# Kernel tuning notes

Measured on AMD Instinct MI355X. Metric: run time of the kernel, lower is better.

The kernel has to match this reference:

```python
import jax, jax.numpy as jnp
import numpy as np

HEADS = 3
NEG_SLOPE = 0.2


def setup_inputs() -> dict:
    key = jax.random.key(0)
    ks = jax.random.split(key, 16)
    B, node_num, his, in_dim = 2, 5000, 12, 2
    N = B * node_num
    E = 160000
    hidden = 32
    C = hidden * his  # 384, per-head out channels of GATConv
    gat_in = in_dim * his  # 24
    s = 0.05
    return {
        "x": jax.random.normal(ks[0], (B, node_num, his, in_dim), jnp.float32),
        "edge_index": jax.random.randint(ks[1], (2, E), 0, N, jnp.int64),
        "lin_w": jax.random.normal(ks[2], (HEADS * C, gat_in), jnp.float32) * s,
        "att_src": jax.random.normal(ks[3], (HEADS, C), jnp.float32) * s,
        "att_dst": jax.random.normal(ks[4], (HEADS, C), jnp.float32) * s,
        "gat_bias": jax.random.normal(ks[5], (C,), jnp.float32) * s,
        "w_ih": jax.random.normal(ks[6], (3 * hidden, hidden), jnp.float32) * s,
        "w_hh": jax.random.normal(ks[7], (3 * hidden, hidden), jnp.float32) * s,
        "b_ih": jax.random.normal(ks[8], (3 * hidden,), jnp.float32) * s,
        "b_hh": jax.random.normal(ks[9], (3 * hidden,), jnp.float32) * s,
        "p1_w": jax.random.normal(ks[10], (1, hidden), jnp.float32) * s,
        "p1_b": jax.random.normal(ks[11], (1,), jnp.float32) * s,
        "p2_w": jax.random.normal(ks[12], (his, his), jnp.float32) * s,
        "p2_b": jax.random.normal(ks[13], (his,), jnp.float32) * s,
    }


def _gat_conv(xf, src, dst, N, lin_w, att_src, att_dst, gat_bias):
    # xf: [N, gat_in]; returns [N, C] (mean over heads, concat=False)
    heads, C = att_src.shape
    h = (xf @ lin_w.T).reshape(N, heads, C)           # [N,heads,C]
    a_src = jnp.einsum('nhc,hc->nh', h, att_src)      # [N,heads]
    a_dst = jnp.einsum('nhc,hc->nh', h, att_dst)
    alpha = jax.nn.leaky_relu(a_src[src] + a_dst[dst], NEG_SLOPE)  # [E,heads]
    # edge softmax over incoming edges of each dst node (stable)
    amax = jax.ops.segment_max(alpha, dst, num_segments=N)
    ea = jnp.exp(alpha - amax[dst])
    denom = jax.ops.segment_sum(ea, dst, num_segments=N)
    w = ea / denom[dst]                               # [E,heads]
    msg = h[src] * w[:, :, None]                      # [E,heads,C] -- dominant traffic
    out = jax.ops.segment_sum(msg, dst, num_segments=N)
    return out.mean(axis=1) + gat_bias                # [N,C]


def _gru(seq, w_ih, w_hh, b_ih, b_hh):
    # seq: [N, T, H] -> outputs [N, T, H], PyTorch GRU gate order (r,z,n)
    N, T, H = seq.shape
    def step(hprev, xt):
        gi = xt @ w_ih.T + b_ih
        gh = hprev @ w_hh.T + b_hh
        ir, iz, inn = jnp.split(gi, 3, axis=-1)
        hr, hz, hn = jnp.split(gh, 3, axis=-1)
        r = jax.nn.sigmoid(ir + hr)
        z = jax.nn.sigmoid(iz + hz)
        n = jnp.tanh(inn + r * hn)
        hnew = (1.0 - z) * n + z * hprev
        return hnew, hnew
    h0 = jnp.zeros((N, H), seq.dtype)
    _, hs = jax.lax.scan(step, h0, seq.transpose(1, 0, 2))
    return hs.transpose(1, 0, 2)


def reference(x, edge_index, lin_w, att_src, att_dst, gat_bias,
              w_ih, w_hh, b_ih, b_hh, p1_w, p1_b, p2_w, p2_b):
    B, node_num, his, in_dim = x.shape
    N = B * node_num
    xf = x.reshape(N, his * in_dim)
    # GATConv adds self-loops (add_self_loops=True default in PyG)
    loops = jnp.arange(N)
    src = jnp.concatenate([edge_index[0], loops])
    dst = jnp.concatenate([edge_index[1], loops])
    gat_out = _gat_conv(xf, src, dst, N, lin_w, att_src, att_dst, gat_bias)  # [N, hidden*his]
    hidden = w_hh.shape[1]
    gru_in = gat_out.reshape(N, his, hidden)
    gru_out = _gru(gru_in, w_ih, w_hh, b_ih, b_hh)    # [N, his, hidden]
    o = (gru_out @ p1_w.T + p1_b).squeeze(-1)         # [N, his]
    o = o @ p2_w.T + p2_b                              # [N, pred_num]
    return o.reshape(B, node_num, -1)
```

## Files before the change

### kernel.cpp

```cpp
#include <hip/hip_runtime.h>
#include <math.h>

#define HEADS 3
#define C_OUT 384
#define GAT_IN 24
#define HID 32
#define TSTEPS 12
#define NEG_SLOPE 0.2f
#define CAPW 64
#define SLOTS 96

typedef __attribute__((ext_vector_type(8))) short bf16x8;
typedef __attribute__((ext_vector_type(4))) float f32x4;

__device__ __forceinline__ float sigm(float x) {
  return 1.f / (1.f + __expf(-x));
}
__device__ __forceinline__ float tanh_fast(float x) {
  return 2.f / (1.f + __expf(-2.f * x)) - 1.f;
}
__device__ __forceinline__ unsigned short f2bf(float x) {
  unsigned int u = __float_as_uint(x);
  unsigned int r = u + 0x7fffu + ((u >> 16) & 1u);
  return (unsigned short)(r >> 16);
}
__device__ __forceinline__ float bf2f(unsigned short u) {
  return __uint_as_float((unsigned int)u << 16);
}
__device__ __forceinline__ float lrelu(float x) {
  return x >= 0.f ? x : NEG_SLOPE * x;
}

__global__ __launch_bounds__(96) void k_const(const float* __restrict__ lin_w,
                                              const float* __restrict__ gat_bias,
                                              const float* __restrict__ wih,
                                              const float* __restrict__ bih,
                                              const float* __restrict__ att_src,
                                              const float* __restrict__ att_dst,
                                              unsigned short* __restrict__ WWt,
                                              float* __restrict__ biasb,
                                              float* __restrict__ vbuf,
                                              int* __restrict__ cnt, int N) {
  int b = blockIdx.x;
  if (b < 876) {
    int t = b / 73, k = b % 73;
    int g = threadIdx.x;
    __shared__ float s_w[32];
    if (g < 32) {
      if (k < 72) {
        int h = k / 24, j = k % 24;
        s_w[g] = lin_w[(size_t)(h * C_OUT + t * 32 + g) * GAT_IN + j] * (1.f / 3.f);
      } else {
        s_w[g] = gat_bias[t * 32 + g];
      }
    }
    __syncthreads();
    const float* wrow = wih + (size_t)g * 32;
    float acc = 0.f;
#pragma unroll
    for (int c = 0; c < 32; ++c) acc += s_w[c] * wrow[c];
    if (k < 72) {
      WWt[((size_t)t * 96 + g) * 96 + k] = f2bf(acc);
      if (k < 24) WWt[((size_t)t * 96 + g) * 96 + 72 + k] = 0;
    } else {
      biasb[t * 96 + g] = acc + bih[g];
    }
  } else if (b < 948) {
    int bb = b - 876;
    int h = bb / 24, j = bb % 24;
    int lane = threadIdx.x;
    if (lane >= 64) return;
    float as = 0.f, ad = 0.f;
    for (int c = lane; c < C_OUT; c += 64) {
      float wv = lin_w[(size_t)(h * C_OUT + c) * GAT_IN + j];
      as += att_src[h * C_OUT + c] * wv;
      ad += att_dst[h * C_OUT + c] * wv;
    }
#pragma unroll
    for (int off = 32; off >= 1; off >>= 1) {
      as += __shfl_xor(as, off, 64);
      ad += __shfl_xor(ad, off, 64);
    }
    if (lane == 0) {
      vbuf[h * 24 + j] = as;
      vbuf[72 + h * 24 + j] = ad;
    }
  } else {
    int i = (b - 948) * 96 + threadIdx.x;
    if (i < N) cnt[i] = 0;
  }
}

__global__ void k_place(const int* __restrict__ esrc,
                        const int* __restrict__ edst, int* __restrict__ cnt,
                        int* __restrict__ slist, int E, int ET) {
  int e = blockIdx.x * blockDim.x + threadIdx.x;
  if (e >= ET) return;
  int d, s;
  if (e < E) { d = edst[e]; s = esrc[e]; }
  else { d = e - E; s = e - E; }
  int pos = atomicAdd(&cnt[d], 1);
  if (pos < SLOTS) slist[(size_t)d * SLOTS + pos] = s;
}

__global__ __launch_bounds__(256) void k_aggx(
    const float* __restrict__ xf, const float* __restrict__ vbuf,
    const int* __restrict__ slist, const int* __restrict__ cnt,
    unsigned short* __restrict__ Yb, int N) {
  __shared__ float s_v[144];
  __shared__ float s_w[4][CAPW][3];
  __shared__ unsigned short s_xb[4][CAPW][26];
  int tid = threadIdx.x, lane = tid & 63, wv = tid >> 6;
  if (tid < 144) s_v[tid] = vbuf[tid];
  __syncthreads();
  int n = blockIdx.x * 4 + wv;
  if (n >= N) return;

  int deg = min(cnt[n], SLOTS);

  float xl = (lane < 24) ? xf[(size_t)n * 24 + lane] : 0.f;
  float ad0, ad1, ad2;
  {
    float p0 = (lane < 24) ? xl * s_v[72 + lane] : 0.f;
    float p1 = (lane < 24) ? xl * s_v[96 + lane] : 0.f;
    float p2 = (lane < 24) ? xl * s_v[120 + lane] : 0.f;
#pragma unroll
    for (int off = 32; off >= 1; off >>= 1) {
      p0 += __shfl_xor(p0, off, 64);
      p1 += __shfl_xor(p1, off, 64);
      p2 += __shfl_xor(p2, off, 64);
    }
    ad0 = p0; ad1 = p1; ad2 = p2;
  }

  float t0 = 0.f, t1 = 0.f, t2 = 0.f;
  for (int i = lane; i < deg; i += 64) {
    int s = slist[(size_t)n * SLOTS + i];
    const float4* xr = (const float4*)(xf + (size_t)s * 24);
    float xs[24];
#pragma unroll
    for (int q = 0; q < 6; ++q) {
      float4 v = xr[q];
      xs[4 * q] = v.x; xs[4 * q + 1] = v.y;
      xs[4 * q + 2] = v.z; xs[4 * q + 3] = v.w;
    }
    float as0 = 0.f, as1 = 0.f, as2 = 0.f;
#pragma unroll
    for (int j = 0; j < 24; ++j) {
      float v = xs[j];
      as0 += v * s_v[j];
      as1 += v * s_v[24 + j];
      as2 += v * s_v[48 + j];
    }
    float e0 = __expf(lrelu(as0 + ad0));
    float e1 = __expf(lrelu(as1 + ad1));
    float e2 = __expf(lrelu(as2 + ad2));
    if (i < CAPW) {
      s_w[wv][i][0] = e0; s_w[wv][i][1] = e1; s_w[wv][i][2] = e2;
#pragma unroll
      for (int j = 0; j < 24; ++j) s_xb[wv][i][j] = f2bf(xs[j]);
    }
    t0 += e0; t1 += e1; t2 += e2;
  }
#pragma unroll
  for (int off = 32; off >= 1; off >>= 1) {
    t0 += __shfl_xor(t0, off, 64);
    t1 += __shfl_xor(t1, off, 64);
    t2 += __shfl_xor(t2, off, 64);
  }
  float inv0 = 1.f / t0, inv1 = 1.f / t1, inv2 = 1.f / t2;

  int eg = lane >> 5;
  int c = lane & 31;
  float acc0 = 0.f, acc1 = 0.f, acc2 = 0.f;
  if (deg <= CAPW) {
    int cc = (c < 24) ? c : 0;
    float cmask = (c < 24) ? 1.f : 0.f;
#pragma unroll 2
    for (int i = eg; i < deg; i += 2) {
      float w0 = s_w[wv][i][0] * inv0;
      float w1 = s_w[wv][i][1] * inv1;
      float w2 = s_w[wv][i][2] * inv2;
      float xv = bf2f(s_xb[wv][i][cc]) * cmask;
      acc0 += w0 * xv; acc1 += w1 * xv; acc2 += w2 * xv;
    }
  } else {
    for (int i = eg; i < deg; i += 2) {
      int s = slist[(size_t)n * SLOTS + i];
      float as0 = 0.f, as1 = 0.f, as2 = 0.f;
      const float* xr = xf + (size_t)s * 24;
#pragma unroll
      for (int j = 0; j < 24; ++j) {
        float v = xr[j];
        as0 += v * s_v[j];
        as1 += v * s_v[24 + j];
        as2 += v * s_v[48 + j];
      }
      float w0 = __expf(lrelu(as0 + ad0)) * inv0;
      float w1 = __expf(lrelu(as1 + ad1)) * inv1;
      float w2 = __expf(lrelu(as2 + ad2)) * inv2;
      float xv = (c < 24) ? xf[(size_t)s * 24 + c] : 0.f;
      acc0 += w0 * xv; acc1 += w1 * xv; acc2 += w2 * xv;
    }
  }
  acc0 += __shfl_xor(acc0, 32, 64);
  acc1 += __shfl_xor(acc1, 32, 64);
  acc2 += __shfl_xor(acc2, 32, 64);
  if (lane < 24) {
    unsigned short* yr = Yb + (size_t)n * 72;
    yr[lane] = f2bf(acc0);
    yr[24 + lane] = f2bf(acc1);
    yr[48 + lane] = f2bf(acc2);
  }
}

__global__ __launch_bounds__(64) void k_rec2(
    const unsigned short* __restrict__ Yb,
    const unsigned short* __restrict__ WWt, const float* __restrict__ biasb,
    const float* __restrict__ whh, const float* __restrict__ bhh,
    const float* __restrict__ p1w, const float* __restrict__ p1b,
    const float* __restrict__ p2w, const float* __restrict__ p2b,
    float* __restrict__ out, int N) {
  __shared__ unsigned short h16[16][32];
  __shared__ float s_o[16][12];
  int l = threadIdx.x;
  int c = l & 15, hi = l >> 4;
  int m0 = blockIdx.x * 16;

  int row = min(m0 + c, N - 1);
  const unsigned short* yr = Yb + (size_t)row * 72;
  bf16x8 ya0 = *(const bf16x8*)(yr + hi * 8);
  bf16x8 ya1 = *(const bf16x8*)(yr + 32 + hi * 8);
  bf16x8 ya2 = {0, 0, 0, 0, 0, 0, 0, 0};
  if (hi == 0) ya2 = *(const bf16x8*)(yr + 64);

  bf16x8 wb[6];
#pragma unroll
  for (int nt = 0; nt < 6; ++nt) {
    const float* wp = whh + (size_t)(nt * 16 + c) * 32 + hi * 8;
#pragma unroll
    for (int j = 0; j < 8; ++j) wb[nt][j] = (short)f2bf(wp[j]);
  }

  float bhr0 = bhh[c], bhr1 = bhh[c + 16];
  float bhz0 = bhh[32 + c], bhz1 = bhh[48 + c];
  float bhn0 = bhh[64 + c], bhn1 = bhh[80 + c];
  float p1c0 = p1w[c], p1c1 = p1w[c + 16], p1b0 = p1b[0];

  float hA[4] = {0.f, 0.f, 0.f, 0.f}, hB[4] = {0.f, 0.f, 0.f, 0.f};
  bf16x8 ha = {0, 0, 0, 0, 0, 0, 0, 0};

  for (int t = 0; t < TSTEPS; ++t) {
    const unsigned short* Wt = WWt + (size_t)t * 96 * 96;
    f32x4 g0 = {0,0,0,0}, g1 = {0,0,0,0}, g2 = {0,0,0,0};
    f32x4 g3 = {0,0,0,0}, g4 = {0,0,0,0}, g5 = {0,0,0,0};
#pragma unroll
    for (int q = 0; q < 3; ++q) {
      bf16x8 aq = (q == 0) ? ya0 : (q == 1) ? ya1 : ya2;
      int ko = q * 32 + hi * 8;
      bf16x8 b0 = *(const bf16x8*)(Wt + (size_t)(0 * 16 + c) * 96 + ko);
      bf16x8 b1 = *(const bf16x8*)(Wt + (size_t)(1 * 16 + c) * 96 + ko);
      bf16x8 b2 = *(const bf16x8*)(Wt + (size_t)(2 * 16 + c) * 96 + ko);
      bf16x8 b3 = *(const bf16x8*)(Wt + (size_t)(3 * 16 + c) * 96 + ko);
      bf16x8 b4 = *(const bf16x8*)(Wt + (size_t)(4 * 16 + c) * 96 + ko);
      bf16x8 b5 = *(const bf16x8*)(Wt + (size_t)(5 * 16 + c) * 96 + ko);
      g0 = __builtin_amdgcn_mfma_f32_16x16x32_bf16(aq, b0, g0, 0, 0, 0);
      g1 = __builtin_amdgcn_mfma_f32_16x16x32_bf16(aq, b1, g1, 0, 0, 0);
      g2 = __builtin_amdgcn_mfma_f32_16x16x32_bf16(aq, b2, g2, 0, 0, 0);
      g3 = __builtin_amdgcn_mfma_f32_16x16x32_bf16(aq, b3, g3, 0, 0, 0);
      g4 = __builtin_amdgcn_mfma_f32_16x16x32_bf16(aq, b4, g4, 0, 0, 0);
      g5 = __builtin_amdgcn_mfma_f32_16x16x32_bf16(aq, b5, g5, 0, 0, 0);
    }
    f32x4 zz = {0,0,0,0};
    f32x4 h0 = __builtin_amdgcn_mfma_f32_16x16x32_bf16(ha, wb[0], zz, 0, 0, 0);
    f32x4 h1 = __builtin_amdgcn_mfma_f32_16x16x32_bf16(ha, wb[1], zz, 0, 0, 0);
    f32x4 h2 = __builtin_amdgcn_mfma_f32_16x16x32_bf16(ha, wb[2], zz, 0, 0, 0);
    f32x4 h3 = __builtin_amdgcn_mfma_f32_16x16x32_bf16(ha, wb[3], zz, 0, 0, 0);
    f32x4 h4 = __builtin_amdgcn_mfma_f32_16x16x32_bf16(ha, wb[4], zz, 0, 0, 0);
    f32x4 h5 = __builtin_amdgcn_mfma_f32_16x16x32_bf16(ha, wb[5], zz, 0, 0, 0);
    const float* bt = biasb + t * 96;
    float br0 = bt[c], br1 = bt[16 + c];
    float bz0 = bt[32 + c], bz1 = bt[48 + c];
    float bn0 = bt[64 + c], bn1 = bt[80 + c];
    float po[4];
#pragma unroll
    for (int reg = 0; reg < 4; ++reg) {
      float r0 = sigm(g0[reg] + br0 + h0[reg] + bhr0);
      float z0 = sigm(g2[reg] + bz0 + h2[reg] + bhz0);
      float n0 = tanh_fast(g4[reg] + bn0 + r0 * (h4[reg] + bhn0));
      hA[reg] = (1.f - z0) * n0 + z0 * hA[reg];
      float r1 = sigm(g1[reg] + br1 + h1[reg] + bhr1);
      float z1 = sigm(g3[reg] + bz1 + h3[reg] + bhz1);
      float n1 = tanh_fast(g5[reg] + bn1 + r1 * (h5[reg] + bhn1));
      hB[reg] = (1.f - z1) * n1 + z1 * hB[reg];
      h16[hi * 4 + reg][c] = f2bf(hA[reg]);
      h16[hi * 4 + reg][c + 16] = f2bf(hB[reg]);
      po[reg] = p1c0 * hA[reg] + p1c1 * hB[reg];
    }
#pragma unroll
    for (int off = 1; off < 16; off <<= 1) {
#pragma unroll
      for (int reg = 0; reg < 4; ++reg) po[reg] += __shfl_xor(po[reg], off, 64);
    }
    if (c == 0) {
#pragma unroll
      for (int reg = 0; reg < 4; ++reg) s_o[hi * 4 + reg][t] = po[reg] + p1b0;
    }
    __syncthreads();
    ha = *(const bf16x8*)&h16[c][hi * 8];
  }
  __syncthreads();
  for (int idx = l; idx < 16 * TSTEPS; idx += 64) {
    int node = idx / TSTEPS, tt = idx % TSTEPS;
    int gn = m0 + node;
    if (gn < N) {
      float acc = p2b[tt];
#pragma unroll
      for (int s2 = 0; s2 < TSTEPS; ++s2)
        acc += p2w[tt * TSTEPS + s2] * s_o[node][s2];
      out[(size_t)gn * TSTEPS + tt] = acc;
    }
  }
}

extern "C" void kernel_launch(void* const* d_in, const int* in_sizes, int n_in,
                              void* d_out, int out_size, void* d_ws,
                              size_t ws_size, hipStream_t stream) {
  const float* x = (const float*)d_in[0];
  const int* ei = (const int*)d_in[1];
  const float* lin_w = (const float*)d_in[2];
  const float* att_src = (const float*)d_in[3];
  const float* att_dst = (const float*)d_in[4];
  const float* gat_bias = (const float*)d_in[5];
  const float* w_ih = (const float*)d_in[6];
  const float* w_hh = (const float*)d_in[7];
  const float* b_ih = (const float*)d_in[8];
  const float* b_hh = (const float*)d_in[9];
  const float* p1w = (const float*)d_in[10];
  const float* p1b = (const float*)d_in[11];
  const float* p2w = (const float*)d_in[12];
  const float* p2b = (const float*)d_in[13];

  int N = in_sizes[0] / GAT_IN;
  int E = in_sizes[1] / 2;
  int ET = E + N;

  size_t off = 0;
  char* base = (char*)d_ws;
  auto alloc = [&](size_t bytes) {
    void* p = base + off;
    off += (bytes + 255) & ~(size_t)255;
    return p;
  };
  unsigned short* Yb = (unsigned short*)alloc((size_t)N * 72 * 2);
  unsigned short* WWt = (unsigned short*)alloc((size_t)12 * 96 * 96 * 2);
  float* biasb = (float*)alloc((size_t)12 * 96 * 4);
  float* vbuf = (float*)alloc(144 * 4);
  int* cnt = (int*)alloc((size_t)N * 4);
  int* slist = (int*)alloc((size_t)N * SLOTS * 4);
  (void)ws_size; (void)n_in; (void)out_size;

  int zero_blocks = (N + 95) / 96;
  k_const<<<948 + zero_blocks, 96, 0, stream>>>(lin_w, gat_bias, w_ih, b_ih,
                                                att_src, att_dst, WWt, biasb,
                                                vbuf, cnt, N);
  k_place<<<(ET + 255) / 256, 256, 0, stream>>>(ei, ei + E, cnt, slist, E, ET);
  k_aggx<<<(N + 3) / 4, 256, 0, stream>>>(x, vbuf, slist, cnt, Yb, N);
  k_rec2<<<(N + 15) / 16, 64, 0, stream>>>(Yb, WWt, biasb, w_hh, b_hh, p1w,
                                           p1b, p2w, p2b, (float*)d_out, N);
}
```

Baseline: 85.35 us.

## Precompute GRU input projections for all timesteps before the recurrence

```diff
diff --git a/kernel.cpp b/kernel.cpp
--- a/kernel.cpp
+++ b/kernel.cpp
@@ -24,6 +24,15 @@
   unsigned int r = u + 0x7fffu + ((u >> 16) & 1u);
   return (unsigned short)(r >> 16);
 }
+__device__ __forceinline__ unsigned int packbf(float lo, float hi) {
+  return (unsigned int)f2bf(lo) | ((unsigned int)f2bf(hi) << 16);
+}
+__device__ __forceinline__ float bf_lo(unsigned int u) {
+  return __uint_as_float(u << 16);
+}
+__device__ __forceinline__ float bf_hi(unsigned int u) {
+  return __uint_as_float(u & 0xffff0000u);
+}
 __device__ __forceinline__ float bf2f(unsigned short u) {
   return __uint_as_float((unsigned int)u << 16);
 }
@@ -37,18 +46,18 @@
                                               const float* __restrict__ bih,
                                               const float* __restrict__ att_src,
                                               const float* __restrict__ att_dst,
-                                              unsigned short* __restrict__ WWt,
+                                              unsigned short* __restrict__ WWf,
                                               float* __restrict__ biasb,
                                               float* __restrict__ vbuf,
                                               int* __restrict__ cnt, int N) {
   int b = blockIdx.x;
   if (b < 876) {
-    int t = b / 73, k = b % 73;
+    int t = b / 73, kk = b % 73;
     int g = threadIdx.x;
     __shared__ float s_w[32];
     if (g < 32) {
-      if (k < 72) {
-        int h = k / 24, j = k % 24;
+      if (kk < 72) {
+        int h = kk / 24, j = kk % 24;
         s_w[g] = lin_w[(size_t)(h * C_OUT + t * 32 + g) * GAT_IN + j] * (1.f / 3.f);
       } else {
         s_w[g] = gat_bias[t * 32 + g];
@@ -59,9 +68,15 @@
     float acc = 0.f;
 #pragma unroll
     for (int c = 0; c < 32; ++c) acc += s_w[c] * wrow[c];
-    if (k < 72) {
-      WWt[((size_t)t * 96 + g) * 96 + k] = f2bf(acc);
-      if (k < 24) WWt[((size_t)t * 96 + g) * 96 + 72 + k] = 0;
+    int nt = g >> 4, c2 = g & 15;
+    if (kk < 72) {
+      int q = kk >> 5, rem = kk & 31, hi2 = rem >> 3, j2 = rem & 7;
+      WWf[((((size_t)t * 3 + q) * 6 + nt) * 64 + hi2 * 16 + c2) * 8 + j2] =
+          f2bf(acc);
+      if (kk < 24) {
+        int remz = kk + 8, hiz = remz >> 3, jz = remz & 7;
+        WWf[((((size_t)t * 3 + 2) * 6 + nt) * 64 + hiz * 16 + c2) * 8 + jz] = 0;
+      }
     } else {
       biasb[t * 96 + g] = acc + bih[g];
     }
@@ -216,16 +231,20 @@
 
 __global__ __launch_bounds__(64) void k_rec2(
     const unsigned short* __restrict__ Yb,
-    const unsigned short* __restrict__ WWt, const float* __restrict__ biasb,
+    const unsigned short* __restrict__ WWf, const float* __restrict__ biasb,
     const float* __restrict__ whh, const float* __restrict__ bhh,
     const float* __restrict__ p1w, const float* __restrict__ p1b,
     const float* __restrict__ p2w, const float* __restrict__ p2b,
     float* __restrict__ out, int N) {
+  __shared__ unsigned int gi_s[12][64][12];
+  __shared__ float s_bias[12][96];
   __shared__ unsigned short h16[16][32];
   __shared__ float s_o[16][12];
   int l = threadIdx.x;
   int c = l & 15, hi = l >> 4;
   int m0 = blockIdx.x * 16;
+
+  for (int u = l; u < 12 * 96; u += 64) s_bias[u / 96][u % 96] = biasb[u];
 
   int row = min(m0 + c, N - 1);
   const unsigned short* yr = Yb + (size_t)row * 72;
@@ -234,36 +253,20 @@
   bf16x8 ya2 = {0, 0, 0, 0, 0, 0, 0, 0};
   if (hi == 0) ya2 = *(const bf16x8*)(yr + 64);
 
-  bf16x8 wb[6];
-#pragma unroll
-  for (int nt = 0; nt < 6; ++nt) {
-    const float* wp = whh + (size_t)(nt * 16 + c) * 32 + hi * 8;
-#pragma unroll
-    for (int j = 0; j < 8; ++j) wb[nt][j] = (short)f2bf(wp[j]);
-  }
-
-  float bhr0 = bhh[c], bhr1 = bhh[c + 16];
-  float bhz0 = bhh[32 + c], bhz1 = bhh[48 + c];
-  float bhn0 = bhh[64 + c], bhn1 = bhh[80 + c];
-  float p1c0 = p1w[c], p1c1 = p1w[c + 16], p1b0 = p1b[0];
-
-  float hA[4] = {0.f, 0.f, 0.f, 0.f}, hB[4] = {0.f, 0.f, 0.f, 0.f};
-  bf16x8 ha = {0, 0, 0, 0, 0, 0, 0, 0};
-
   for (int t = 0; t < TSTEPS; ++t) {
-    const unsigned short* Wt = WWt + (size_t)t * 96 * 96;
     f32x4 g0 = {0,0,0,0}, g1 = {0,0,0,0}, g2 = {0,0,0,0};
     f32x4 g3 = {0,0,0,0}, g4 = {0,0,0,0}, g5 = {0,0,0,0};
 #pragma unroll
     for (int q = 0; q < 3; ++q) {
       bf16x8 aq = (q == 0) ? ya0 : (q == 1) ? ya1 : ya2;
-      int ko = q * 32 + hi * 8;
-      bf16x8 b0 = *(const bf16x8*)(Wt + (size_t)(0 * 16 + c) * 96 + ko);
-      bf16x8 b1 = *(const bf16x8*)(Wt + (size_t)(1 * 16 + c) * 96 + ko);
-      bf16x8 b2 = *(const bf16x8*)(Wt + (size_t)(2 * 16 + c) * 96 + ko);
-      bf16x8 b3 = *(const bf16x8*)(Wt + (size_t)(3 * 16 + c) * 96 + ko);
-      bf16x8 b4 = *(const bf16x8*)(Wt + (size_t)(4 * 16 + c) * 96 + ko);
-      bf16x8 b5 = *(const bf16x8*)(Wt + (size_t)(5 * 16 + c) * 96 + ko);
+      const unsigned short* bp =
+          WWf + ((((size_t)t * 3 + q) * 6) * 64 + l) * 8;
+      bf16x8 b0 = *(const bf16x8*)(bp + 0 * 512);
+      bf16x8 b1 = *(const bf16x8*)(bp + 1 * 512);
+      bf16x8 b2 = *(const bf16x8*)(bp + 2 * 512);
+      bf16x8 b3 = *(const bf16x8*)(bp + 3 * 512);
+      bf16x8 b4 = *(const bf16x8*)(bp + 4 * 512);
+      bf16x8 b5 = *(const bf16x8*)(bp + 5 * 512);
       g0 = __builtin_amdgcn_mfma_f32_16x16x32_bf16(aq, b0, g0, 0, 0, 0);
       g1 = __builtin_amdgcn_mfma_f32_16x16x32_bf16(aq, b1, g1, 0, 0, 0);
       g2 = __builtin_amdgcn_mfma_f32_16x16x32_bf16(aq, b2, g2, 0, 0, 0);
@@ -271,27 +274,62 @@
       g4 = __builtin_amdgcn_mfma_f32_16x16x32_bf16(aq, b4, g4, 0, 0, 0);
       g5 = __builtin_amdgcn_mfma_f32_16x16x32_bf16(aq, b5, g5, 0, 0, 0);
     }
-    f32x4 zz = {0,0,0,0};
+    unsigned int* gp = &gi_s[t][l][0];
+    gp[0] = packbf(g0[0], g0[1]);  gp[1] = packbf(g0[2], g0[3]);
+    gp[2] = packbf(g1[0], g1[1]);  gp[3] = packbf(g1[2], g1[3]);
+    gp[4] = packbf(g2[0], g2[1]);  gp[5] = packbf(g2[2], g2[3]);
+    gp[6] = packbf(g3[0], g3[1]);  gp[7] = packbf(g3[2], g3[3]);
+    gp[8] = packbf(g4[0], g4[1]);  gp[9] = packbf(g4[2], g4[3]);
+    gp[10] = packbf(g5[0], g5[1]); gp[11] = packbf(g5[2], g5[3]);
+  }
+
+  bf16x8 wb[6];
+#pragma unroll
+  for (int nt = 0; nt < 6; ++nt) {
+    const float* wp = whh + (size_t)(nt * 16 + c) * 32 + hi * 8;
+#pragma unroll
+    for (int j = 0; j < 8; ++j) wb[nt][j] = (short)f2bf(wp[j]);
+  }
+
+  float bhr0 = bhh[c], bhr1 = bhh[c + 16];
+  float bhz0 = bhh[32 + c], bhz1 = bhh[48 + c];
+  float bhn0 = bhh[64 + c], bhn1 = bhh[80 + c];
+  float p1c0 = p1w[c], p1c1 = p1w[c + 16], p1b0 = p1b[0];
+
+  float hA[4] = {0.f, 0.f, 0.f, 0.f}, hB[4] = {0.f, 0.f, 0.f, 0.f};
+  bf16x8 ha = {0, 0, 0, 0, 0, 0, 0, 0};
+
+  for (int t = 0; t < TSTEPS; ++t) {
+    uint4 va = *(const uint4*)&gi_s[t][l][0];
+    uint4 vb = *(const uint4*)&gi_s[t][l][4];
+    uint4 vc = *(const uint4*)&gi_s[t][l][8];
+    f32x4 zz = {0, 0, 0, 0};
     f32x4 h0 = __builtin_amdgcn_mfma_f32_16x16x32_bf16(ha, wb[0], zz, 0, 0, 0);
     f32x4 h1 = __builtin_amdgcn_mfma_f32_16x16x32_bf16(ha, wb[1], zz, 0, 0, 0);
     f32x4 h2 = __builtin_amdgcn_mfma_f32_16x16x32_bf16(ha, wb[2], zz, 0, 0, 0);
     f32x4 h3 = __builtin_amdgcn_mfma_f32_16x16x32_bf16(ha, wb[3], zz, 0, 0, 0);
     f32x4 h4 = __builtin_amdgcn_mfma_f32_16x16x32_bf16(ha, wb[4], zz, 0, 0, 0);
     f32x4 h5 = __builtin_amdgcn_mfma_f32_16x16x32_bf16(ha, wb[5], zz, 0, 0, 0);
-    const float* bt = biasb + t * 96;
+    const float* bt = &s_bias[t][0];
     float br0 = bt[c], br1 = bt[16 + c];
     float bz0 = bt[32 + c], bz1 = bt[48 + c];
     float bn0 = bt[64 + c], bn1 = bt[80 + c];
+    float g0v[4] = {bf_lo(va.x), bf_hi(va.x), bf_lo(va.y), bf_hi(va.y)};
+    float g1v[4] = {bf_lo(va.z), bf_hi(va.z), bf_lo(va.w), bf_hi(va.w)};
+    float g2v[4] = {bf_lo(vb.x), bf_hi(vb.x), bf_lo(vb.y), bf_hi(vb.y)};
+    float g3v[4] = {bf_lo(vb.z), bf_hi(vb.z), bf_lo(vb.w), bf_hi(vb.w)};
+    float g4v[4] = {bf_lo(vc.x), bf_hi(vc.x), bf_lo(vc.y), bf_hi(vc.y)};
+    float g5v[4] = {bf_lo(vc.z), bf_hi(vc.z), bf_lo(vc.w), bf_hi(vc.w)};
     float po[4];
 #pragma unroll
     for (int reg = 0; reg < 4; ++reg) {
-      float r0 = sigm(g0[reg] + br0 + h0[reg] + bhr0);
-      float z0 = sigm(g2[reg] + bz0 + h2[reg] + bhz0);
-      float n0 = tanh_fast(g4[reg] + bn0 + r0 * (h4[reg] + bhn0));
+      float r0 = sigm(g0v[reg] + br0 + h0[reg] + bhr0);
+      float z0 = sigm(g2v[reg] + bz0 + h2[reg] + bhz0);
+      float n0 = tanh_fast(g4v[reg] + bn0 + r0 * (h4[reg] + bhn0));
       hA[reg] = (1.f - z0) * n0 + z0 * hA[reg];
-      float r1 = sigm(g1[reg] + br1 + h1[reg] + bhr1);
-      float z1 = sigm(g3[reg] + bz1 + h3[reg] + bhz1);
-      float n1 = tanh_fast(g5[reg] + bn1 + r1 * (h5[reg] + bhn1));
+      float r1 = sigm(g1v[reg] + br1 + h1[reg] + bhr1);
+      float z1 = sigm(g3v[reg] + bz1 + h3[reg] + bhz1);
+      float n1 = tanh_fast(g5v[reg] + bn1 + r1 * (h5[reg] + bhn1));
       hB[reg] = (1.f - z1) * n1 + z1 * hB[reg];
       h16[hi * 4 + reg][c] = f2bf(hA[reg]);
       h16[hi * 4 + reg][c + 16] = f2bf(hB[reg]);
@@ -353,7 +391,7 @@
     return p;
   };
   unsigned short* Yb = (unsigned short*)alloc((size_t)N * 72 * 2);
-  unsigned short* WWt = (unsigned short*)alloc((size_t)12 * 96 * 96 * 2);
+  unsigned short* WWf = (unsigned short*)alloc((size_t)12 * 3 * 6 * 64 * 8 * 2);
   float* biasb = (float*)alloc((size_t)12 * 96 * 4);
   float* vbuf = (float*)alloc(144 * 4);
   int* cnt = (int*)alloc((size_t)N * 4);
@@ -362,10 +400,10 @@
 
   int zero_blocks = (N + 95) / 96;
   k_const<<<948 + zero_blocks, 96, 0, stream>>>(lin_w, gat_bias, w_ih, b_ih,
-                                                att_src, att_dst, WWt, biasb,
+                                                att_src, att_dst, WWf, biasb,
                                                 vbuf, cnt, N);
   k_place<<<(ET + 255) / 256, 256, 0, stream>>>(ei, ei + E, cnt, slist, E, ET);
   k_aggx<<<(N + 3) / 4, 256, 0, stream>>>(x, vbuf, slist, cnt, Yb, N);
-  k_rec2<<<(N + 15) / 16, 64, 0, stream>>>(Yb, WWt, biasb, w_hh, b_hh, p1w,
+  k_rec2<<<(N + 15) / 16, 64, 0, stream>>>(Yb, WWf, biasb, w_hh, b_hh, p1w,
                                            p1b, p2w, p2b, (float*)d_out, N);
 }
```

New measurement: 79.25 us. -7.1%, faster.
